# Kernel tuning notes

Hardware: AMD Instinct MI355X
Metric: run time of the kernel (lower is better)

Reference implementation:

```python
import functools
import jax, jax.numpy as jnp
import numpy as np

N_WIRES = 8
NUM_BLOCK = 3
P_BITFLIP = 0.02
P_DEPOL = 0.03
BATCH = 64
C = jnp.complex64


def _const_kraus():
    I = np.eye(2)
    X = np.array([[0.0, 1.0], [1.0, 0.0]])
    Y = np.array([[0.0, -1j], [1j, 0.0]])
    Z = np.diag([1.0, -1.0])
    bf = np.stack([np.sqrt(1 - P_BITFLIP) * I, np.sqrt(P_BITFLIP) * X]).astype(np.complex64)
    dp = np.stack([
        np.sqrt(1 - P_DEPOL) * I,
        np.sqrt(P_DEPOL / 3) * X,
        np.sqrt(P_DEPOL / 3) * Y,
        np.sqrt(P_DEPOL / 3) * Z,
    ]).astype(np.complex64)
    return jnp.asarray(bf), jnp.asarray(dp)

BITFLIP_K, DEPOL_K = _const_kraus()


def rot_mat(phi, theta, omega):
    # PennyLane Rot(phi, theta, omega) = RZ(omega) RY(theta) RZ(phi)
    c = jnp.cos(theta / 2).astype(C)
    s = jnp.sin(theta / 2).astype(C)
    ep = jnp.exp(-0.5j * (phi + omega).astype(C))  # e^{-i(phi+omega)/2}
    em = jnp.exp(-0.5j * (phi - omega).astype(C))  # e^{-i(phi-omega)/2}
    return jnp.stack([
        jnp.stack([ep * c, -jnp.conj(em) * s]),
        jnp.stack([em * s, jnp.conj(ep) * c]),
    ])


def amp_damp_kraus(g):
    g = g.astype(C)
    z = jnp.zeros((), C)
    o = jnp.ones((), C)
    K0 = jnp.stack([jnp.stack([o, z]), jnp.stack([z, jnp.sqrt(1 - g)])])
    K1 = jnp.stack([jnp.stack([z, jnp.sqrt(g)]), jnp.stack([z, z])])
    return jnp.stack([K0, K1])


def _apply_axis(rho, M, axis):
    # contract 2x2 matrix M into the given tensor axis of rho
    r = jnp.tensordot(M, rho, axes=([1], [axis]))
    return jnp.moveaxis(r, 0, axis)


def apply_channel(rho, Ks, wire):
    # rho' = sum_k K_k rho K_k^dagger on one wire (ket axis=wire, bra axis=N+wire)
    out = 0.0
    for k in range(Ks.shape[0]):
        r = _apply_axis(rho, Ks[k], wire)
        r = _apply_axis(r, jnp.conj(Ks[k]), N_WIRES + wire)
        out = out + r
    return out

_CZ_SGN = jnp.array([[1.0, 1.0], [1.0, -1.0]], C)


def apply_cz(rho, j):
    # CZ is diagonal: multiply by (-1)^{a&b} on ket pair and bra pair
    shape = [1] * (2 * N_WIRES)
    shape[j] = 2
    shape[j + 1] = 2
    rho = rho * _CZ_SGN.reshape(shape)
    shape = [1] * (2 * N_WIRES)
    shape[N_WIRES + j] = 2
    shape[N_WIRES + j + 1] = 2
    return rho * _CZ_SGN.reshape(shape)


def _wire_step(rho, x3, w3, wire):
    rho = apply_channel(rho, rot_mat(x3[0], x3[1], x3[2])[None], wire)
    rho = apply_channel(rho, rot_mat(w3[0], w3[1], w3[2])[None], wire)
    rho = apply_channel(rho, BITFLIP_K, wire)
    rho = apply_channel(rho, DEPOL_K, wire)
    g = jax.nn.sigmoid(x3[0])  # deterministic choice (source uses random.randint(0,2) pick)
    rho = apply_channel(rho, amp_damp_kraus(g), wire)
    return rho


def simulate(xr, w):
    n = N_WIRES
    rho = jnp.zeros((2,) * (2 * n), C).at[(0,) * (2 * n)].set(1.0)
    for blk in range(NUM_BLOCK):
        for i in range(n):
            step = jax.checkpoint(functools.partial(_wire_step, wire=i))
            rho = step(rho, xr[3 * i:3 * i + 3], w[blk, i])
        if NUM_BLOCK > 1 and blk < NUM_BLOCK - 1:
            for j in range(n - 1):
                rho = apply_cz(rho, j)
            # source applies trailing noise to last loop wire i = n_wires-1
            rho = apply_channel(rho, BITFLIP_K, n - 1)
            rho = apply_channel(rho, DEPOL_K, n - 1)
    dim = 2 ** n
    probs = jnp.diagonal(rho.reshape(dim, dim)).real.reshape((2,) * n)
    z = jnp.array([1.0, -1.0], probs.dtype)
    return jnp.stack([jnp.sum(jnp.tensordot(probs, z, axes=([i], [0]))) for i in range(n)])


def setup_inputs() -> dict:
    key = jax.random.key(0)
    kx, kw = jax.random.split(key)
    x = jax.random.normal(kx, (BATCH, 3 * N_WIRES), jnp.float32)
    weights = jax.random.uniform(kw, (NUM_BLOCK, N_WIRES, 3), jnp.float32, 0.0, 2.0 * np.pi)
    return {"x": x, "weights": weights}


def reference(x, weights):
    return jax.vmap(lambda xr: simulate(xr, weights))(x)  # [B, n_wires]
```

## Files before the change

kernel.cpp:

```cpp
#include <hip/hip_runtime.h>
#include <math.h>

namespace {

constexpr float P_BF = 0.02f;
constexpr float P_DP = 0.03f;

__device__ inline void rot3(float ph, float th, float om, float R[3][3]){
  float sp,cp,st,ct,so,co;
  sincosf(ph,&sp,&cp); sincosf(th,&st,&ct); sincosf(om,&so,&co);
  R[0][0]= co*ct*cp - so*sp; R[0][1]= -co*ct*sp - so*cp; R[0][2]= co*st;
  R[1][0]= so*ct*cp + co*sp; R[1][1]= -so*ct*sp + co*cp; R[1][2]= so*st;
  R[2][0]= -st*cp;           R[2][1]=  st*sp;            R[2][2]= ct;
}

__device__ inline void wire_ptm(const float* __restrict__ x3,
                                const float* __restrict__ w3,
                                float M[4][4]){
  float Rx[3][3], Rw[3][3], R[3][3];
  rot3(x3[0],x3[1],x3[2],Rx);
  rot3(w3[0],w3[1],w3[2],Rw);
  #pragma unroll
  for (int i=0;i<3;++i)
    #pragma unroll
    for (int j=0;j<3;++j)
      R[i][j] = Rw[i][0]*Rx[0][j] + Rw[i][1]*Rx[1][j] + Rw[i][2]*Rx[2][j];
  float g  = 1.f/(1.f+expf(-x3[0]));
  float sq = sqrtf(fmaxf(1.f-g,0.f));
  const float c = 1.f - 4.f*P_DP/3.f;
  const float b = 1.f - 2.f*P_BF;
  M[0][0]=1.f; M[0][1]=0.f; M[0][2]=0.f; M[0][3]=0.f;
  M[1][0]=0.f; M[2][0]=0.f; M[3][0]=g;
  #pragma unroll
  for (int j=0;j<3;++j){
    M[1][j+1] = sq*c*R[0][j];
    M[2][j+1] = sq*c*b*R[1][j];
    M[3][j+1] = (1.f-g)*c*b*R[2][j];
  }
}

__global__ __launch_bounds__(64) void pqc_ptm(const float* __restrict__ xg,
                                              const float* __restrict__ wgt,
                                              float* __restrict__ outg){
  const int tid = (int)blockIdx.x*64 + (int)threadIdx.x;
  const int r = tid>>3, iw = tid&7;
  const float* xr = xg + r*24;

  const float cdp = 1.f - 4.f*P_DP/3.f;
  const float bbf = 1.f - 2.f*P_BF;
  const float nd1 = cdp, nd2 = cdp*bbf, nd3 = cdp*bbf;

  const bool has_l = iw>=1, has_r = iw<=6;
  const bool cz_s0 = iw>=2, cz_s1 = has_l, cz_s2 = has_r, cz_s3 = iw<=5;
  const int wl  = has_l ? iw-1 : 0;
  const int wr  = has_r ? iw+1 : 7;
  const int wll = cz_s0 ? iw-2 : 0;
  const int wrr = cz_s3 ? iw+2 : 7;

  float M[4][4];

  wire_ptm(xr+3*iw, wgt+(16+iw)*3, M);
  float a1[4] = {M[3][0], M[3][1], M[3][2], M[3][3]};
  if (iw==7){ a1[1]*=nd1; a1[2]*=nd2; a1[3]*=nd3; }

  float Mb[4][4];
  wire_ptm(xr+3*iw, wgt+(8+iw)*3, Mb);
  wire_ptm(xr+3*wl, wgt+(8+wl)*3, M);
  float L[4];
  #pragma unroll
  for (int x=0;x<4;++x) L[x] = has_l ? M[3][x] : (x==0?1.f:0.f);
  wire_ptm(xr+3*wr, wgt+(8+wr)*3, M);
  float Rv[4];
  #pragma unroll
  for (int z=0;z<4;++z) Rv[z] = has_r ? M[3][z] : (z==0?1.f:0.f);

  float A[4], B[4];
  #pragma unroll
  for (int y=0;y<4;++y){
    A[y] = a1[0]*Mb[0][y] + a1[3]*Mb[3][y];
    B[y] = a1[1]*Mb[1][y] + a1[2]*Mb[2][y];
  }
  B[0] = 0.f;

  if (iw==7){
    A[1]*=nd1; A[2]*=nd2; A[3]*=nd3;
    B[1]*=nd1; B[2]*=nd2; B[3]*=nd3;
  }
  if (iw==6){
    Rv[1]*=nd1; Rv[2]*=nd2; Rv[3]*=nd3;
  }

  float m1[4], m2[4], m3[4], m0z, m4z;
  wire_ptm(xr+3*iw, wgt+iw*3, M);
  #pragma unroll
  for (int q=0;q<4;++q) m2[q] = M[q][0]+M[q][3];
  wire_ptm(xr+3*wl, wgt+wl*3, M);
  #pragma unroll
  for (int q=0;q<4;++q) m1[q] = M[q][0]+M[q][3];
  wire_ptm(xr+3*wr, wgt+wr*3, M);
  #pragma unroll
  for (int q=0;q<4;++q) m3[q] = M[q][0]+M[q][3];
  wire_ptm(xr+3*wll, wgt+wll*3, M);
  m0z = M[3][0]+M[3][3];
  wire_ptm(xr+3*wrr, wgt+wrr*3, M);
  m4z = M[3][0]+M[3][3];

  float out = 0.f;

  #pragma unroll
  for (int p2=0;p2<4;++p2){
    float t = A[p2]*m2[p2];
    if (p2==1||p2==2){
      t *= cz_s1 ? m1[3] : 1.f;
      t *= cz_s2 ? m3[3] : 1.f;
    }
    out += t;
  }

  #pragma unroll
  for (int p1=0;p1<4;++p1){
    const bool in1 = (p1==1)||(p1==2);
    const float v0 = (cz_s0 && in1) ? m0z : 1.f;
    const float lp = L[p1]*v0;
    #pragma unroll
    for (int p2=1;p2<4;++p2){
      const bool in2 = (p2==1)||(p2==2);
      const float q1v  = (cz_s1 && in2) ? m1[p1^3] : m1[p1];
      const bool  f1   = cz_s1 && in1;
      const float sgn1 = (cz_s1 && in1 && in2 && (p1!=p2)) ? -1.f : 1.f;
      const float base = lp * B[p2] * q1v * sgn1;
      #pragma unroll
      for (int p3=0;p3<4;++p3){
        const bool in3 = (p3==1)||(p3==2);
        const float v4 = (cz_s3 && in3) ? m4z : 1.f;
        const bool  f2 = cz_s2 && in3;
        const float q2v = (f1!=f2) ? m2[p2^3] : m2[p2];
        const float q3v = (cz_s2 && in2) ? m3[p3^3] : m3[p3];
        const bool  neq = f1 ? ((p2^3)!=p3) : (p2!=p3);
        const float sgn2 = (cz_s2 && in2 && in3 && neq) ? -1.f : 1.f;
        out += base * Rv[p3] * v4 * q2v * q3v * sgn2;
      }
    }
  }

  outg[r*8+iw] = out;
}

}

extern "C" void kernel_launch(void* const* d_in, const int* in_sizes, int n_in,
                              void* d_out, int out_size, void* d_ws, size_t ws_size,
                              hipStream_t stream) {
  (void)in_sizes; (void)n_in; (void)d_ws; (void)ws_size; (void)out_size;
  const float* x = (const float*)d_in[0];
  const float* w = (const float*)d_in[1];
  float* out = (float*)d_out;
  pqc_ptm<<<dim3(8), dim3(64), 0, stream>>>(x, w, out);
}
```

Measured before the change: 12.01 us.

## Compute each wire transfer matrix once per row and share via LDS

Each thread used to recompute up to ten per-wire Pauli transfer matrices, with sincos, exp and sqrt, for its neighbours, so the same matrices were evaluated many times. Now each batch row gets its own block. 24 threads each compute one (block, wire) matrix into shared memory, and after a barrier 8 threads run the contraction from those shared values. This removes the redundant transcendental work and shortens the per-thread serial chain. The cost is a __syncthreads, 64 blocks in which most lanes sit idle, and extra shared-memory reads.

```diff
diff --git a/kernel.cpp b/kernel.cpp
--- a/kernel.cpp
+++ b/kernel.cpp
@@ -39,111 +39,113 @@
   }
 }
 
-__global__ __launch_bounds__(64) void pqc_ptm(const float* __restrict__ xg,
-                                              const float* __restrict__ wgt,
-                                              float* __restrict__ outg){
-  const int tid = (int)blockIdx.x*64 + (int)threadIdx.x;
-  const int r = tid>>3, iw = tid&7;
+__global__ __launch_bounds__(64) void pqc_ptm2(const float* __restrict__ xg,
+                                               const float* __restrict__ wgt,
+                                               float* __restrict__ outg){
+  __shared__ float Ms[3][8][4][4];
+  const int r = (int)blockIdx.x;
+  const int t = (int)threadIdx.x;
   const float* xr = xg + r*24;
 
-  const float cdp = 1.f - 4.f*P_DP/3.f;
-  const float bbf = 1.f - 2.f*P_BF;
-  const float nd1 = cdp, nd2 = cdp*bbf, nd3 = cdp*bbf;
+  if (t < 24){
+    const int blk = t>>3, wire = t&7;
+    float M[4][4];
+    wire_ptm(xr + 3*wire, wgt + (blk*8 + wire)*3, M);
+    #pragma unroll
+    for (int a=0;a<4;++a)
+      #pragma unroll
+      for (int b=0;b<4;++b) Ms[blk][wire][a][b] = M[a][b];
+  }
+  __syncthreads();
 
-  const bool has_l = iw>=1, has_r = iw<=6;
-  const bool cz_s0 = iw>=2, cz_s1 = has_l, cz_s2 = has_r, cz_s3 = iw<=5;
-  const int wl  = has_l ? iw-1 : 0;
-  const int wr  = has_r ? iw+1 : 7;
-  const int wll = cz_s0 ? iw-2 : 0;
-  const int wrr = cz_s3 ? iw+2 : 7;
+  if (t < 8){
+    const int iw = t;
+    const float cdp = 1.f - 4.f*P_DP/3.f;
+    const float bbf = 1.f - 2.f*P_BF;
+    const float nd1 = cdp, nd2 = cdp*bbf, nd3 = cdp*bbf;
 
-  float M[4][4];
+    const bool has_l = iw>=1, has_r = iw<=6;
+    const bool cz_s0 = iw>=2, cz_s1 = has_l, cz_s2 = has_r, cz_s3 = iw<=5;
+    const int wl  = has_l ? iw-1 : 0;
+    const int wr  = has_r ? iw+1 : 7;
+    const int wll = cz_s0 ? iw-2 : 0;
+    const int wrr = cz_s3 ? iw+2 : 7;
 
-  wire_ptm(xr+3*iw, wgt+(16+iw)*3, M);
-  float a1[4] = {M[3][0], M[3][1], M[3][2], M[3][3]};
-  if (iw==7){ a1[1]*=nd1; a1[2]*=nd2; a1[3]*=nd3; }
+    float a1[4];
+    #pragma unroll
+    for (int q=0;q<4;++q) a1[q] = Ms[2][iw][3][q];
+    if (iw==7){ a1[1]*=nd1; a1[2]*=nd2; a1[3]*=nd3; }
 
-  float Mb[4][4];
-  wire_ptm(xr+3*iw, wgt+(8+iw)*3, Mb);
-  wire_ptm(xr+3*wl, wgt+(8+wl)*3, M);
-  float L[4];
-  #pragma unroll
-  for (int x=0;x<4;++x) L[x] = has_l ? M[3][x] : (x==0?1.f:0.f);
-  wire_ptm(xr+3*wr, wgt+(8+wr)*3, M);
-  float Rv[4];
-  #pragma unroll
-  for (int z=0;z<4;++z) Rv[z] = has_r ? M[3][z] : (z==0?1.f:0.f);
+    float L[4], Rv[4];
+    #pragma unroll
+    for (int q=0;q<4;++q){
+      L[q]  = has_l ? Ms[1][wl][3][q] : (q==0?1.f:0.f);
+      Rv[q] = has_r ? Ms[1][wr][3][q] : (q==0?1.f:0.f);
+    }
+    float A[4], B[4];
+    #pragma unroll
+    for (int y=0;y<4;++y){
+      A[y] = a1[0]*Ms[1][iw][0][y] + a1[3]*Ms[1][iw][3][y];
+      B[y] = a1[1]*Ms[1][iw][1][y] + a1[2]*Ms[1][iw][2][y];
+    }
+    B[0] = 0.f;
 
-  float A[4], B[4];
-  #pragma unroll
-  for (int y=0;y<4;++y){
-    A[y] = a1[0]*Mb[0][y] + a1[3]*Mb[3][y];
-    B[y] = a1[1]*Mb[1][y] + a1[2]*Mb[2][y];
-  }
-  B[0] = 0.f;
+    if (iw==7){
+      A[1]*=nd1; A[2]*=nd2; A[3]*=nd3;
+      B[1]*=nd1; B[2]*=nd2; B[3]*=nd3;
+    }
+    if (iw==6){ Rv[1]*=nd1; Rv[2]*=nd2; Rv[3]*=nd3; }
 
-  if (iw==7){
-    A[1]*=nd1; A[2]*=nd2; A[3]*=nd3;
-    B[1]*=nd1; B[2]*=nd2; B[3]*=nd3;
-  }
-  if (iw==6){
-    Rv[1]*=nd1; Rv[2]*=nd2; Rv[3]*=nd3;
-  }
+    float m1[4], m2[4], m3[4];
+    #pragma unroll
+    for (int q=0;q<4;++q){
+      m2[q] = Ms[0][iw][q][0] + Ms[0][iw][q][3];
+      m1[q] = Ms[0][wl][q][0] + Ms[0][wl][q][3];
+      m3[q] = Ms[0][wr][q][0] + Ms[0][wr][q][3];
+    }
+    const float m0z = Ms[0][wll][3][0] + Ms[0][wll][3][3];
+    const float m4z = Ms[0][wrr][3][0] + Ms[0][wrr][3][3];
 
-  float m1[4], m2[4], m3[4], m0z, m4z;
-  wire_ptm(xr+3*iw, wgt+iw*3, M);
-  #pragma unroll
-  for (int q=0;q<4;++q) m2[q] = M[q][0]+M[q][3];
-  wire_ptm(xr+3*wl, wgt+wl*3, M);
-  #pragma unroll
-  for (int q=0;q<4;++q) m1[q] = M[q][0]+M[q][3];
-  wire_ptm(xr+3*wr, wgt+wr*3, M);
-  #pragma unroll
-  for (int q=0;q<4;++q) m3[q] = M[q][0]+M[q][3];
-  wire_ptm(xr+3*wll, wgt+wll*3, M);
-  m0z = M[3][0]+M[3][3];
-  wire_ptm(xr+3*wrr, wgt+wrr*3, M);
-  m4z = M[3][0]+M[3][3];
+    float out = 0.f;
 
-  float out = 0.f;
+    #pragma unroll
+    for (int p2=0;p2<4;++p2){
+      float tv = A[p2]*m2[p2];
+      if (p2==1||p2==2){
+        tv *= cz_s1 ? m1[3] : 1.f;
+        tv *= cz_s2 ? m3[3] : 1.f;
+      }
+      out += tv;
+    }
 
-  #pragma unroll
-  for (int p2=0;p2<4;++p2){
-    float t = A[p2]*m2[p2];
-    if (p2==1||p2==2){
-      t *= cz_s1 ? m1[3] : 1.f;
-      t *= cz_s2 ? m3[3] : 1.f;
-    }
-    out += t;
-  }
-
-  #pragma unroll
-  for (int p1=0;p1<4;++p1){
-    const bool in1 = (p1==1)||(p1==2);
-    const float v0 = (cz_s0 && in1) ? m0z : 1.f;
-    const float lp = L[p1]*v0;
     #pragma unroll
-    for (int p2=1;p2<4;++p2){
-      const bool in2 = (p2==1)||(p2==2);
-      const float q1v  = (cz_s1 && in2) ? m1[p1^3] : m1[p1];
-      const bool  f1   = cz_s1 && in1;
-      const float sgn1 = (cz_s1 && in1 && in2 && (p1!=p2)) ? -1.f : 1.f;
-      const float base = lp * B[p2] * q1v * sgn1;
+    for (int p1=0;p1<4;++p1){
+      const bool in1 = (p1==1)||(p1==2);
+      const float v0 = (cz_s0 && in1) ? m0z : 1.f;
+      const float lp = L[p1]*v0;
       #pragma unroll
-      for (int p3=0;p3<4;++p3){
-        const bool in3 = (p3==1)||(p3==2);
-        const float v4 = (cz_s3 && in3) ? m4z : 1.f;
-        const bool  f2 = cz_s2 && in3;
-        const float q2v = (f1!=f2) ? m2[p2^3] : m2[p2];
-        const float q3v = (cz_s2 && in2) ? m3[p3^3] : m3[p3];
-        const bool  neq = f1 ? ((p2^3)!=p3) : (p2!=p3);
-        const float sgn2 = (cz_s2 && in2 && in3 && neq) ? -1.f : 1.f;
-        out += base * Rv[p3] * v4 * q2v * q3v * sgn2;
+      for (int p2=1;p2<4;++p2){
+        const bool in2 = (p2==1)||(p2==2);
+        const float q1v  = (cz_s1 && in2) ? m1[p1^3] : m1[p1];
+        const bool  f1   = cz_s1 && in1;
+        const float sgn1 = (cz_s1 && in1 && in2 && (p1!=p2)) ? -1.f : 1.f;
+        const float base = lp * B[p2] * q1v * sgn1;
+        #pragma unroll
+        for (int p3=0;p3<4;++p3){
+          const bool in3 = (p3==1)||(p3==2);
+          const float v4 = (cz_s3 && in3) ? m4z : 1.f;
+          const bool  f2 = cz_s2 && in3;
+          const float q2v = (f1!=f2) ? m2[p2^3] : m2[p2];
+          const float q3v = (cz_s2 && in2) ? m3[p3^3] : m3[p3];
+          const bool  neq = f1 ? ((p2^3)!=p3) : (p2!=p3);
+          const float sgn2 = (cz_s2 && in2 && in3 && neq) ? -1.f : 1.f;
+          out += base * Rv[p3] * v4 * q2v * q3v * sgn2;
+        }
       }
     }
+
+    outg[r*8 + iw] = out;
   }
-
-  outg[r*8+iw] = out;
 }
 
 }
@@ -155,5 +157,5 @@
   const float* x = (const float*)d_in[0];
   const float* w = (const float*)d_in[1];
   float* out = (float*)d_out;
-  pqc_ptm<<<dim3(8), dim3(64), 0, stream>>>(x, w, out);
+  pqc_ptm2<<<dim3(64), dim3(64), 0, stream>>>(x, w, out);
 }
```

Result: faster. 9.631 us (-19.8%).
